# Performance work log

Measured on AMD Instinct MI355X. Metric: run time of the kernel, lower is better.

Reference implementation:

```python
import jax, jax.numpy as jnp
import numpy as np

N_NODES = 10000
N_EDGES = 160000
N_GRAPHS = 20
IN_F, HID, OUT_F, HEADS = 50, 256, 121, 4
NEG_SLOPE = 0.2
GN_EPS = 1e-5
SM_EPS = 1e-16


def _with_self_loops(edge_index, n):
    loop = jnp.arange(n, dtype=edge_index.dtype)
    src = jnp.concatenate([edge_index[0], loop])
    dst = jnp.concatenate([edge_index[1], loop])
    return src, dst


def gat_conv(x, W, att_src, att_dst, bias, src, dst, heads, out_c):
    # PyG GATConv: linear -> per-node attention halves -> edge leaky_relu
    # -> softmax over incoming edges of each dst -> weighted scatter-sum.
    n = x.shape[0]
    h = (x @ W).reshape(n, heads, out_c)                # [N,H,C]
    a_s = (h * att_src).sum(-1)                          # [N,H]
    a_d = (h * att_dst).sum(-1)                          # [N,H]
    e = a_s[src] + a_d[dst]                              # [E,H]
    e = jnp.where(e > 0, e, NEG_SLOPE * e)
    e_max = jax.ops.segment_max(e, dst, num_segments=n)  # self-loops cover all dst
    ex = jnp.exp(e - e_max[dst])
    den = jax.ops.segment_sum(ex, dst, num_segments=n)
    alpha = ex / (den[dst] + SM_EPS)                     # [E,H]
    out = jax.ops.segment_sum(h[src] * alpha[..., None], dst, num_segments=n)
    return out.reshape(n, heads * out_c) + bias


def graph_norm(x, batch, weight, bias, mean_scale, n_graphs):
    cnt = jax.ops.segment_sum(jnp.ones((x.shape[0],), x.dtype), batch,
                              num_segments=n_graphs)[:, None]    # [G,1]
    mean = jax.ops.segment_sum(x, batch, num_segments=n_graphs) / cnt
    ctr = x - mean[batch] * mean_scale
    var = jax.ops.segment_sum(ctr * ctr, batch, num_segments=n_graphs) / cnt
    inv = jax.lax.rsqrt(var + GN_EPS)
    return weight * ctr * inv[batch] + bias


def setup_inputs() -> dict:
    key = jax.random.key(0)
    ks = jax.random.split(key, 24)
    d = {}
    d['x'] = jax.random.normal(ks[0], (N_NODES, IN_F), jnp.float32)
    d['edge_index'] = jax.random.randint(ks[1], (2, N_EDGES), 0, N_NODES, jnp.int64 if jax.config.jax_enable_x64 else jnp.int32)
    d['batch'] = jnp.sort(jax.random.randint(ks[2], (N_NODES,), 0, N_GRAPHS))
    def glorot(k, shape):
        fan = shape[0] + shape[-1]
        return jax.random.normal(k, shape, jnp.float32) * np.sqrt(2.0 / fan)
    dims = [(IN_F, HEADS, HID), (HEADS * HID, HEADS, HID), (HEADS * HID, HEADS, HID), (HEADS * HID, 1, OUT_F)]
    i = 3
    for li, (fin, h, c) in enumerate(dims, 1):
        d[f'W{li}'] = glorot(ks[i], (fin, h * c)); i += 1
        d[f'as{li}'] = glorot(ks[i], (h, c)); i += 1
        d[f'ad{li}'] = glorot(ks[i], (h, c)); i += 1
        d[f'b{li}'] = jnp.zeros((h * c,), jnp.float32)
    for li in (1, 2, 3):
        w = HEADS * HID
        d[f'gw{li}'] = jnp.ones((w,), jnp.float32)
        d[f'gb{li}'] = jnp.zeros((w,), jnp.float32)
        d[f'ga{li}'] = jnp.ones((w,), jnp.float32)
    return d


def reference(x, edge_index, batch,
              W1, as1, ad1, b1, W2, as2, ad2, b2, W3, as3, ad3, b3, W4, as4, ad4, b4,
              gw1, gb1, ga1, gw2, gb2, ga2, gw3, gb3, ga3):
    src, dst = _with_self_loops(edge_index, N_NODES)
    h = gat_conv(x, W1, as1, ad1, b1, src, dst, HEADS, HID)
    h = jax.nn.elu(graph_norm(h, batch, gw1, gb1, ga1, N_GRAPHS))
    h = gat_conv(h, W2, as2, ad2, b2, src, dst, HEADS, HID)
    h = jax.nn.elu(graph_norm(h, batch, gw2, gb2, ga2, N_GRAPHS))
    h = gat_conv(h, W3, as3, ad3, b3, src, dst, HEADS, HID)
    h = jax.nn.elu(graph_norm(h, batch, gw3, gb3, ga3, N_GRAPHS))
    return gat_conv(h, W4, as4, ad4, b4, src, dst, 1, OUT_F)
```

## Files before the change

### kernel.cpp

```cpp
#include <hip/hip_runtime.h>
#include <math.h>

#define NN 10000
#define NE 160000
#define E2 (NE + NN)
#define NG 20
#define MPAD 10240
#define NSPLIT 8

typedef __attribute__((ext_vector_type(8))) short short8;
typedef __attribute__((ext_vector_type(4))) float f32x4;
typedef __attribute__((ext_vector_type(4))) unsigned short us4;

__device__ inline unsigned short f2bf(float f){
  unsigned u = __float_as_uint(f);
  unsigned r = u + 0x7FFFu + ((u >> 16) & 1u);
  return (unsigned short)(r >> 16);
}
__device__ inline float bf2f(unsigned short h){ return __uint_as_float(((unsigned)h) << 16); }

__device__ inline void gload_lds16(const void* g, void* l){
  __builtin_amdgcn_global_load_lds((const __attribute__((address_space(1))) void*)g,
                                   (__attribute__((address_space(3))) void*)l, 16, 0, 0);
}

__global__ void k_gptr(const int* __restrict__ batch, int* __restrict__ gptr){
  int g = threadIdx.x;
  if (g > NG) return;
  int lo = 0, hi = NN;
  while (lo < hi){ int mid = (lo+hi)>>1; if (batch[mid] < g) lo = mid+1; else hi = mid; }
  gptr[g] = lo;
}

__global__ void k_count(const int* __restrict__ ei, int* __restrict__ cnt){
  int e = blockIdx.x*256 + threadIdx.x;
  if (e >= E2) return;
  int d = (e < NE) ? ei[NE + e] : (e - NE);
  atomicAdd(&cnt[d], 1);
}

__global__ void k_scan(const int* __restrict__ cnt, int* __restrict__ ptr){
  __shared__ int tpre[256];
  __shared__ int tsum[256];
  int tid = threadIdx.x;
  const int per = (NN + 255)/256;
  int base = tid*per;
  int s = 0;
  for (int i=0;i<per;i++){ int idx=base+i; if (idx<NN) s += cnt[idx]; }
  tsum[tid] = s;
  __syncthreads();
  if (tid == 0){
    int run = 0;
    for (int i=0;i<256;i++){ tpre[i]=run; run += tsum[i]; }
    ptr[NN] = run;
  }
  __syncthreads();
  int run = tpre[tid];
  for (int i=0;i<per;i++){ int idx=base+i; if (idx<NN){ ptr[idx]=run; run += cnt[idx]; } }
}

__global__ void k_copy(const int* __restrict__ src, int* __restrict__ dst){
  int i = blockIdx.x*256 + threadIdx.x;
  if (i < NN) dst[i] = src[i];
}

__global__ void k_scatter(const int* __restrict__ ei, int* __restrict__ fill, int* __restrict__ csrc){
  int e = blockIdx.x*256 + threadIdx.x;
  if (e >= E2) return;
  int s, d;
  if (e < NE){ s = ei[e]; d = ei[NE + e]; } else { s = d = e - NE; }
  int pos = atomicAdd(&fill[d], 1);
  csrc[pos] = s;
}

__global__ void k_xconv(const float* __restrict__ x, unsigned short* __restrict__ xbf){
  int i = blockIdx.x*256 + threadIdx.x;
  if (i >= MPAD*64) return;
  int r = i >> 6, c = i & 63;
  float v = (r < NN && c < 50) ? x[r*50 + c] : 0.f;
  xbf[i] = f2bf(v);
}

#define WT0 0
#define WT1 65536
#define WT2 1114112
#define WT3 2162688
#define WTT 2293760
__global__ void k_wconvall(const float* __restrict__ W0, const float* __restrict__ W1,
                           const float* __restrict__ W2, const float* __restrict__ W3,
                           unsigned short* __restrict__ wt){
  int i = blockIdx.x*256 + threadIdx.x;
  if (i >= WTT) return;
  const float* W; int K, N, Kpad, off;
  if (i < WT1){ W=W0; K=50; N=1024; Kpad=64; off=WT0; }
  else if (i < WT2){ W=W1; K=1024; N=1024; Kpad=1024; off=WT1; }
  else if (i < WT3){ W=W2; K=1024; N=1024; Kpad=1024; off=WT2; }
  else { W=W3; K=1024; N=121; Kpad=1024; off=WT3; }
  int j = i - off;
  int nn = j / Kpad, kk = j - nn*Kpad;
  float v = (nn < N && kk < K) ? W[(size_t)kk*N + nn] : 0.f;
  wt[i] = f2bf(v);
}

__global__ void k_attpad4(const float* __restrict__ AS3, const float* __restrict__ AD3,
                          float* __restrict__ asp4, float* __restrict__ adp4){
  int i = threadIdx.x;
  asp4[i] = (i < 121) ? AS3[i] : 0.f;
  adp4[i] = (i < 121) ? AD3[i] : 0.f;
}

template<int TBM, int TBN>
__global__ __launch_bounds__(512, 4) void k_gemm256(
    const unsigned short* __restrict__ A,
    const unsigned short* __restrict__ Bt,
    unsigned short* __restrict__ Cbf,
    const float* __restrict__ asp, const float* __restrict__ adp,
    float* __restrict__ a_s, float* __restrict__ a_d,
    int M, int K, int FS, int ncb, int H)
{
  constexpr int MFR = TBM/32;
  constexpr int NFR = TBN/64;
  constexpr int ABYTES = TBM*64;
  constexpr int BBYTES = TBN*64;
  constexpr int AINST = TBM/128;
  constexpr int BINST = TBN/128;
  constexpr int LPS = AINST + BINST;
  __shared__ unsigned short sA[3*TBM*32];
  __shared__ unsigned short sB[3*TBN*32];
  const int tid = threadIdx.x;
  const int wave = tid >> 6;
  const int lane = tid & 63;
  const int nwg = gridDim.x;
  const int q = nwg >> 3, rmod = nwg & 7;
  const int xcd = blockIdx.x & 7, idx = blockIdx.x >> 3;
  const int wg = (xcd < rmod) ? (xcd*(q+1) + idx) : (rmod*(q+1) + (xcd - rmod)*q + idx);
  const int rowt = wg / ncb;
  const int colt = wg - rowt*ncb;
  const int row0 = rowt * TBM;
  const int col0 = colt * TBN;
  const int wr = (wave >> 2) * (TBM/2);
  const int wc = (wave & 3) * (TBN/4);
  f32x4 acc[MFR][NFR];
  #pragma unroll
  for (int i=0;i<MFR;i++)
    #pragma unroll
    for (int j=0;j<NFR;j++){ acc[i][j][0]=0.f; acc[i][j][1]=0.f; acc[i][j][2]=0.f; acc[i][j][3]=0.f; }

  const unsigned short* aP[AINST];
  int aL[AINST];
  #pragma unroll
  for (int i=0;i<AINST;i++){
    int s = (wave*AINST + i)*64 + lane;
    int row = s >> 2, chn = (s & 3) ^ ((row >> 1) & 3);
    aP[i] = A + (size_t)(row0 + row)*K + chn*8;
    aL[i] = (wave*AINST + i)*1024;
  }
  const unsigned short* bP[BINST];
  int bL[BINST];
  #pragma unroll
  for (int i=0;i<BINST;i++){
    int s = (wave*BINST + i)*64 + lane;
    int row = s >> 2, chn = (s & 3) ^ ((row >> 1) & 3);
    bP[i] = Bt + (size_t)(col0 + row)*K + chn*8;
    bL[i] = (wave*BINST + i)*1024;
  }
  char* ldsA = (char*)sA;
  char* ldsB = (char*)sB;

  auto STAGE = [&](int k0, int buf){
    #pragma unroll
    for (int i=0;i<AINST;i++) gload_lds16(aP[i] + k0, ldsA + buf*ABYTES + aL[i]);
    #pragma unroll
    for (int i=0;i<BINST;i++) gload_lds16(bP[i] + k0, ldsB + buf*BBYTES + bL[i]);
  };

  const int NT = K >> 5;
  const int kch = lane >> 4;
  const int rlo = lane & 15;

  STAGE(0, 0);
  STAGE(32, 1);

  int cur = 0;
  for (int t = 0; t < NT; ++t){
    asm volatile("s_waitcnt lgkmcnt(0)" ::: "memory");
    if (t+1 < NT){
      if constexpr (LPS==4)      asm volatile("s_waitcnt vmcnt(4)" ::: "memory");
      else if constexpr (LPS==3) asm volatile("s_waitcnt vmcnt(3)" ::: "memory");
      else                       asm volatile("s_waitcnt vmcnt(2)" ::: "memory");
    } else {
      asm volatile("s_waitcnt vmcnt(0)" ::: "memory");
    }
    __builtin_amdgcn_sched_barrier(0);
    __builtin_amdgcn_s_barrier();
    __builtin_amdgcn_sched_barrier(0);
    const unsigned short* bA = sA + cur*(TBM*32);
    const unsigned short* bB = sB + cur*(TBN*32);
    short8 af[MFR], bfr[NFR];
    #pragma unroll
    for (int m=0;m<MFR;m++){
      int r = wr + m*16 + rlo;
      af[m] = *(const short8*)(bA + r*32 + ((kch ^ ((r>>1)&3))<<3));
    }
    #pragma unroll
    for (int n=0;n<NFR;n++){
      int r = wc + n*16 + rlo;
      bfr[n] = *(const short8*)(bB + r*32 + ((kch ^ ((r>>1)&3))<<3));
    }
    if (t+2 < NT){
      int nb = cur + 2; if (nb >= 3) nb -= 3;
      STAGE((t+2) << 5, nb);
    }
    __builtin_amdgcn_s_setprio(1);
    #pragma unroll
    for (int m=0;m<MFR;m++)
      #pragma unroll
      for (int n=0;n<NFR;n++)
        acc[m][n] = __builtin_amdgcn_mfma_f32_16x16x32_bf16(af[m], bfr[n], acc[m][n], 0, 0, 0);
    __builtin_amdgcn_s_setprio(0);
    cur += 1; if (cur == 3) cur = 0;
  }
  const int cr = (lane >> 4) * 4;
  const int cc = lane & 15;
  #pragma unroll
  for (int m=0;m<MFR;m++){
    #pragma unroll
    for (int n=0;n<NFR;n++){
      int col = col0 + wc + n*16 + cc;
      #pragma unroll
      for (int r=0;r<4;r++){
        int row = row0 + wr + m*16 + cr + r;
        if (row < M) Cbf[(size_t)row*FS + col] = f2bf(acc[m][n][r]);
      }
    }
  }
  float asv[NFR], adv[NFR];
  #pragma unroll
  for (int n=0;n<NFR;n++){
    int col = col0 + wc + n*16 + cc;
    asv[n] = asp[col]; adv[n] = adp[col];
  }
  __syncthreads();
  float* part = (float*)sA;
  #pragma unroll
  for (int m=0;m<MFR;m++){
    #pragma unroll
    for (int r=0;r<4;r++){
      float ss = 0.f, sd = 0.f;
      #pragma unroll
      for (int n=0;n<NFR;n++){ float v = acc[m][n][r]; ss += v*asv[n]; sd += v*adv[n]; }
      #pragma unroll
      for (int o=8;o;o>>=1){ ss += __shfl_xor(ss,o); sd += __shfl_xor(sd,o); }
      if (cc == 0){
        int rowLocal = m*16 + cr + r;
        int pidx = ((wave>>2)*(TBM/2) + rowLocal)*8 + (wave&3)*2;
        part[pidx] = ss; part[pidx+1] = sd;
      }
    }
  }
  __syncthreads();
  if (tid < TBM*2){
    int row = tid >> 1, v = tid & 1;
    int base = row*8 + v;
    float s = part[base] + part[base+2] + part[base+4] + part[base+6];
    int grow = row0 + row;
    const int head = colt;
    if (grow < M){
      if (v) a_d[grow*H + head] = s;
      else   a_s[grow*H + head] = s;
    }
  }
}

__global__ __launch_bounds__(256) void k_gatherw(
    const unsigned short* __restrict__ h,
    const float* __restrict__ a_s, const float* __restrict__ a_d,
    const int* __restrict__ ptr, const int* __restrict__ csrc,
    const float* __restrict__ bias, float* __restrict__ out)
{
  __shared__ float sal[4][64*4];
  __shared__ int ssn[4][64];
  const int wid = threadIdx.x >> 6, lane = threadIdx.x & 63;
  const int node = blockIdx.x*4 + wid;
  const int hh = lane >> 4;
  const int beg = ptr[node], deg = ptr[node+1] - beg;
  f32x4 ad4 = *(const f32x4*)(a_d + node*4);
  float acc[16], acc2[16];
  #pragma unroll
  for (int j=0;j<16;j++){ acc[j]=0.f; acc2[j]=0.f; }
  f32x4 denp = {0.f,0.f,0.f,0.f};
  const unsigned short* hb = h + lane*16;

  for (int c0 = 0; c0 < deg; c0 += 64){
    int n = min(64, deg - c0);
    if (lane < n){
      int s = csrc[beg + c0 + lane];
      f32x4 as4 = *(const f32x4*)(a_s + s*4);
      f32x4 e4;
      #pragma unroll
      for (int k2=0;k2<4;k2++){
        float ev = as4[k2] + ad4[k2];
        ev = ev > 0.f ? ev : 0.2f*ev;
        float x = __expf(ev);
        e4[k2] = x;
        denp[k2] += x;
      }
      *(f32x4*)&sal[wid][lane*4] = e4;
      ssn[wid][lane] = s;
    }
    int e = 0;
    if (n >= 2){
      int s0 = ssn[wid][0], s1 = ssn[wid][1];
      float aA = sal[wid][hh], aB = sal[wid][4+hh];
      const unsigned short* p0 = hb + (size_t)s0*1024;
      const unsigned short* p1 = hb + (size_t)s1*1024;
      short8 ca0=*(const short8*)p0, ca1=*(const short8*)(p0+8);
      short8 cb0=*(const short8*)p1, cb1=*(const short8*)(p1+8);
      for (e = 0; e+3 < n; e += 2){
        int s2 = ssn[wid][e+2], s3 = ssn[wid][e+3];
        float nA = sal[wid][(e+2)*4+hh], nB = sal[wid][(e+3)*4+hh];
        const unsigned short* p2 = hb + (size_t)s2*1024;
        const unsigned short* p3 = hb + (size_t)s3*1024;
        short8 na0=*(const short8*)p2, na1=*(const short8*)(p2+8);
        short8 nb0=*(const short8*)p3, nb1=*(const short8*)(p3+8);
        #pragma unroll
        for (int j=0;j<8;j++){ acc[j]   += bf2f((unsigned short)ca0[j])*aA;
                               acc[8+j] += bf2f((unsigned short)ca1[j])*aA; }
        #pragma unroll
        for (int j=0;j<8;j++){ acc2[j]   += bf2f((unsigned short)cb0[j])*aB;
                               acc2[8+j] += bf2f((unsigned short)cb1[j])*aB; }
        ca0=na0; ca1=na1; cb0=nb0; cb1=nb1; aA=nA; aB=nB;
      }
      #pragma unroll
      for (int j=0;j<8;j++){ acc[j]   += bf2f((unsigned short)ca0[j])*aA;
                             acc[8+j] += bf2f((unsigned short)ca1[j])*aA; }
      #pragma unroll
      for (int j=0;j<8;j++){ acc2[j]   += bf2f((unsigned short)cb0[j])*aB;
                             acc2[8+j] += bf2f((unsigned short)cb1[j])*aB; }
      e += 2;
    }
    for (; e < n; ++e){
      int s = ssn[wid][e];
      float al = sal[wid][e*4 + hh];
      const unsigned short* p = hb + (size_t)s*1024;
      short8 u0 = *(const short8*)p, u1 = *(const short8*)(p+8);
      #pragma unroll
      for (int j=0;j<8;j++){ acc[j]   += bf2f((unsigned short)u0[j])*al;
                             acc[8+j] += bf2f((unsigned short)u1[j])*al; }
    }
  }
  #pragma unroll
  for (int o=32;o;o>>=1){
    #pragma unroll
    for (int k2=0;k2<4;k2++) denp[k2] += __shfl_xor(denp[k2], o);
  }
  float inv = 1.f / (denp[hh] + 1e-16f);
  float* op = out + (size_t)node*1024 + lane*16;
  const float* bp = bias + lane*16;
  #pragma unroll
  for (int j=0;j<16;j++) op[j] = (acc[j]+acc2[j])*inv + bp[j];
}

__global__ __launch_bounds__(256) void k_gatherw1(
    const unsigned short* __restrict__ h,
    const float* __restrict__ a_s, const float* __restrict__ a_d,
    const int* __restrict__ ptr, const int* __restrict__ csrc,
    const float* __restrict__ bias, float* __restrict__ out)
{
  __shared__ float sal[4][64];
  __shared__ int ssn[4][64];
  const int wid = threadIdx.x >> 6, lane = threadIdx.x & 63;
  const int node = blockIdx.x*4 + wid;
  const int beg = ptr[node], deg = ptr[node+1] - beg;
  float ad = a_d[node];
  float den = 0.f;
  float acc[2] = {0.f,0.f}, acc2[2] = {0.f,0.f};
  const int c0i = lane*2;
  const unsigned short* hb = h + c0i;

  for (int b0 = 0; b0 < deg; b0 += 64){
    int n = min(64, deg - b0);
    if (lane < n){
      int s = csrc[beg + b0 + lane];
      float ev = a_s[s] + ad;
      ev = ev > 0.f ? ev : 0.2f*ev;
      float x = __expf(ev);
      sal[wid][lane] = x;
      ssn[wid][lane] = s;
      den += x;
    }
    int e = 0;
    for (; e + 1 < n; e += 2){
      int sA_ = ssn[wid][e], sB_ = ssn[wid][e+1];
      float aA = sal[wid][e], aB = sal[wid][e+1];
      const unsigned short* pA = hb + (size_t)sA_*128;
      const unsigned short* pB = hb + (size_t)sB_*128;
      acc[0]  += bf2f(pA[0])*aA; acc[1]  += bf2f(pA[1])*aA;
      acc2[0] += bf2f(pB[0])*aB; acc2[1] += bf2f(pB[1])*aB;
    }
    if (e < n){
      int sA_ = ssn[wid][e];
      float aA = sal[wid][e];
      const unsigned short* pA = hb + (size_t)sA_*128;
      acc[0] += bf2f(pA[0])*aA; acc[1] += bf2f(pA[1])*aA;
    }
  }
  #pragma unroll
  for (int o=32;o;o>>=1) den += __shfl_xor(den, o);
  float inv = 1.f / (den + 1e-16f);
  if (c0i < 121)   out[(size_t)node*121 + c0i]   = (acc[0]+acc2[0])*inv + bias[c0i];
  if (c0i+1 < 121) out[(size_t)node*121 + c0i+1] = (acc[1]+acc2[1])*inv + bias[c0i+1];
}

__global__ void k_gnstats(const float* __restrict__ x, const int* __restrict__ gptr,
                          float* __restrict__ psum, float* __restrict__ psq){
  int g = blockIdx.x, sp = blockIdx.z;
  int c4 = threadIdx.x*4;
  int beg = gptr[g], end = gptr[g+1];
  int n = end - beg;
  int per = (n + NSPLIT - 1) / NSPLIT;
  int nb = beg + sp*per, ne = min(end, nb + per);
  f32x4 s = {0.f,0.f,0.f,0.f}, qv = {0.f,0.f,0.f,0.f};
  for (int i = nb; i < ne; i++){
    f32x4 v = *(const f32x4*)(x + (size_t)i*1024 + c4);
    s += v; qv += v*v;
  }
  int idx = (sp*NG + g)*1024 + c4;
  *(f32x4*)(psum + idx) = s;
  *(f32x4*)(psq + idx) = qv;
}

__global__ void k_coef(const float* __restrict__ psum, const float* __restrict__ psq,
                       const int* __restrict__ gptr,
                       const float* __restrict__ w, const float* __restrict__ b, const float* __restrict__ ms,
                       float* __restrict__ cA, float* __restrict__ cB){
  int i = blockIdx.x*256 + threadIdx.x;
  if (i >= NG*1024) return;
  int g = i >> 10, c = i & 1023;
  float cntf = (float)(gptr[g+1] - gptr[g]);
  float sm = 0.f, sq = 0.f;
  #pragma unroll
  for (int sp=0; sp<NSPLIT; sp++){
    sm += psum[(sp*NG + g)*1024 + c];
    sq += psq[(sp*NG + g)*1024 + c];
  }
  float m = sm / cntf;
  float s = ms[c];
  float ex2 = sq / cntf;
  float var = ex2 - 2.f*s*m*m + s*s*m*m;
  float inv = rsqrtf(var + 1e-5f);
  float wa = w[c]*inv;
  cA[i] = wa;
  cB[i] = b[c] - wa*m*s;
}

__global__ void k_applyelu(const float* __restrict__ x, const int* __restrict__ batch,
                           const float* __restrict__ cA, const float* __restrict__ cB,
                           unsigned short* __restrict__ obf){
  int i = blockIdx.x*256 + threadIdx.x;
  if (i >= NN*256) return;
  int node = i >> 8;
  int c4 = (i & 255)*4;
  int g = batch[node];
  f32x4 v = *(const f32x4*)(x + (size_t)node*1024 + c4);
  f32x4 a = *(const f32x4*)(cA + g*1024 + c4);
  f32x4 b = *(const f32x4*)(cB + g*1024 + c4);
  us4 o;
  #pragma unroll
  for (int j=0;j<4;j++){
    float y = a[j]*v[j] + b[j];
    y = y > 0.f ? y : expm1f(y);
    o[j] = f2bf(y);
  }
  *(us4*)(obf + (size_t)node*1024 + c4) = o;
}

extern "C" void kernel_launch(void* const* d_in, const int* in_sizes, int n_in,
                              void* d_out, int out_size, void* d_ws, size_t ws_size,
                              hipStream_t stream){
  (void)in_sizes; (void)n_in; (void)out_size; (void)ws_size;
  const float* x     = (const float*)d_in[0];
  const int*   ei    = (const int*)d_in[1];
  const int*   batch = (const int*)d_in[2];
  const float* W[4]  = {(const float*)d_in[3],  (const float*)d_in[7],  (const float*)d_in[11], (const float*)d_in[15]};
  const float* AS[4] = {(const float*)d_in[4],  (const float*)d_in[8],  (const float*)d_in[12], (const float*)d_in[16]};
  const float* AD[4] = {(const float*)d_in[5],  (const float*)d_in[9],  (const float*)d_in[13], (const float*)d_in[17]};
  const float* BI[4] = {(const float*)d_in[6],  (const float*)d_in[10], (const float*)d_in[14], (const float*)d_in[18]};
  const float* GW[3] = {(const float*)d_in[19], (const float*)d_in[22], (const float*)d_in[25]};
  const float* GB[3] = {(const float*)d_in[20], (const float*)d_in[23], (const float*)d_in[26]};
  const float* GA[3] = {(const float*)d_in[21], (const float*)d_in[24], (const float*)d_in[27]};

  float* ws   = (float*)d_ws;
  float* bufB = ws;
  float* a_s  = bufB + (size_t)NN*1024;
  float* a_d  = a_s + (size_t)NN*4;
  float* psum = a_d + (size_t)NN*4;
  float* psq  = psum + (size_t)NSPLIT*NG*1024;
  float* cA   = psq  + (size_t)NSPLIT*NG*1024;
  float* cB   = cA   + (size_t)NG*1024;
  float* asp4 = cB   + (size_t)NG*1024;
  float* adp4 = asp4 + 128;
  int* ptr  = (int*)(adp4 + 128);
  int* fill = ptr + (NN + 8);
  int* csrc = fill + (NN + 8);
  int* gptr = csrc + E2;
  unsigned short* abf = (unsigned short*)(gptr + 24);
  unsigned short* xbf = abf;
  unsigned short* hbf = abf + (size_t)MPAD*1024;
  unsigned short* wt  = hbf + (size_t)NN*1024;

  hipMemsetAsync(fill, 0, sizeof(int)*(NN+1), stream);
  k_gptr<<<1, 32, 0, stream>>>(batch, gptr);
  k_count<<<(E2+255)/256, 256, 0, stream>>>(ei, fill);
  k_scan<<<1, 256, 0, stream>>>(fill, ptr);
  k_copy<<<(NN+255)/256, 256, 0, stream>>>(ptr, fill);
  k_scatter<<<(E2+255)/256, 256, 0, stream>>>(ei, fill, csrc);
  k_xconv<<<(MPAD*64+255)/256, 256, 0, stream>>>(x, xbf);
  k_wconvall<<<(WTT+255)/256, 256, 0, stream>>>(W[0], W[1], W[2], W[3], wt);
  k_attpad4<<<1, 128, 0, stream>>>(AS[3], AD[3], asp4, adp4);

  const int Kp[4]  = {64, 1024, 1024, 1024};
  const int Np[4]  = {1024, 1024, 1024, 128};
  const int Woff[4] = {WT0, WT1, WT2, WT3};
  for (int li = 0; li < 4; ++li){
    int FS = Np[li];
    const unsigned short* Ain = (li == 0) ? xbf : abf;
    const unsigned short* Wt = wt + Woff[li];
    if (li < 3){
      int ncb = 4;
      int nwg = (MPAD/128) * ncb;
      k_gemm256<128,256><<<nwg, 512, 0, stream>>>(Ain, Wt, hbf, AS[li], AD[li], a_s, a_d,
                                                  NN, Kp[li], FS, ncb, 4);
      k_gatherw<<<NN/4, 256, 0, stream>>>(hbf, a_s, a_d, ptr, csrc, BI[li], bufB);
      k_gnstats<<<dim3(NG, 1, NSPLIT), 256, 0, stream>>>(bufB, gptr, psum, psq);
      k_coef<<<(NG*1024 + 255)/256, 256, 0, stream>>>(psum, psq, gptr, GW[li], GB[li], GA[li], cA, cB);
      k_applyelu<<<(NN*256 + 255)/256, 256, 0, stream>>>(bufB, batch, cA, cB, abf);
    } else {
      int ncb = 1;
      int nwg = (MPAD/256) * ncb;
      k_gemm256<256,128><<<nwg, 512, 0, stream>>>(Ain, Wt, hbf, asp4, adp4, a_s, a_d,
                                                  NN, Kp[li], FS, ncb, 1);
      k_gatherw1<<<NN/4, 256, 0, stream>>>(hbf, a_s, a_d, ptr, csrc, BI[li], (float*)d_out);
    }
  }
}
```

Measured before the change: 482.4 us.

## Merge setup kernels, shrink last-layer GEMM tile, widen gather loads, more GN splits

Folds the x conversion, weight conversion and attention padding kernels into one setup launch to cut launch overhead. The final layer GEMM moves to a 128x128 tile so twice as many workgroups cover the 10240 padded rows. The layer-4 gather reads two bf16 values with one 32-bit load instead of two 16-bit loads. The GraphNorm stats split goes from 8 to 16 to raise parallelism. The 128x128 template instantiation is untested here and may interact differently with the GEMM epilogue.

After: 445.5 us. 1.08x faster.

```diff
diff --git a/kernel.cpp b/kernel.cpp
--- a/kernel.cpp
+++ b/kernel.cpp
@@ -6,7 +6,7 @@
 #define E2 (NE + NN)
 #define NG 20
 #define MPAD 10240
-#define NSPLIT 8
+#define NSPLIT 16
 
 typedef __attribute__((ext_vector_type(8))) short short8;
 typedef __attribute__((ext_vector_type(4))) float f32x4;
@@ -73,40 +73,39 @@
   csrc[pos] = s;
 }
 
-__global__ void k_xconv(const float* __restrict__ x, unsigned short* __restrict__ xbf){
-  int i = blockIdx.x*256 + threadIdx.x;
-  if (i >= MPAD*64) return;
-  int r = i >> 6, c = i & 63;
-  float v = (r < NN && c < 50) ? x[r*50 + c] : 0.f;
-  xbf[i] = f2bf(v);
-}
-
 #define WT0 0
 #define WT1 65536
 #define WT2 1114112
 #define WT3 2162688
 #define WTT 2293760
-__global__ void k_wconvall(const float* __restrict__ W0, const float* __restrict__ W1,
-                           const float* __restrict__ W2, const float* __restrict__ W3,
-                           unsigned short* __restrict__ wt){
+#define XS  (MPAD*64)
+__global__ void k_setup(const float* __restrict__ W0, const float* __restrict__ W1,
+                        const float* __restrict__ W2, const float* __restrict__ W3,
+                        const float* __restrict__ x,
+                        const float* __restrict__ AS3, const float* __restrict__ AD3,
+                        unsigned short* __restrict__ wt, unsigned short* __restrict__ xbf,
+                        float* __restrict__ asp4, float* __restrict__ adp4){
   int i = blockIdx.x*256 + threadIdx.x;
-  if (i >= WTT) return;
-  const float* W; int K, N, Kpad, off;
-  if (i < WT1){ W=W0; K=50; N=1024; Kpad=64; off=WT0; }
-  else if (i < WT2){ W=W1; K=1024; N=1024; Kpad=1024; off=WT1; }
-  else if (i < WT3){ W=W2; K=1024; N=1024; Kpad=1024; off=WT2; }
-  else { W=W3; K=1024; N=121; Kpad=1024; off=WT3; }
-  int j = i - off;
-  int nn = j / Kpad, kk = j - nn*Kpad;
-  float v = (nn < N && kk < K) ? W[(size_t)kk*N + nn] : 0.f;
-  wt[i] = f2bf(v);
-}
-
-__global__ void k_attpad4(const float* __restrict__ AS3, const float* __restrict__ AD3,
-                          float* __restrict__ asp4, float* __restrict__ adp4){
-  int i = threadIdx.x;
-  asp4[i] = (i < 121) ? AS3[i] : 0.f;
-  adp4[i] = (i < 121) ? AD3[i] : 0.f;
+  if (i < WTT){
+    const float* W; int K, N, Kpad, off;
+    if (i < WT1){ W=W0; K=50; N=1024; Kpad=64; off=WT0; }
+    else if (i < WT2){ W=W1; K=1024; N=1024; Kpad=1024; off=WT1; }
+    else if (i < WT3){ W=W2; K=1024; N=1024; Kpad=1024; off=WT2; }
+    else { W=W3; K=1024; N=121; Kpad=1024; off=WT3; }
+    int j = i - off;
+    int nn = j / Kpad, kk = j - nn*Kpad;
+    float v = (nn < N && kk < K) ? W[(size_t)kk*N + nn] : 0.f;
+    wt[i] = f2bf(v);
+  } else if (i < WTT + XS){
+    int j = i - WTT;
+    int r = j >> 6, c = j & 63;
+    float v = (r < NN && c < 50) ? x[r*50 + c] : 0.f;
+    xbf[j] = f2bf(v);
+  } else if (i < WTT + XS + 128){
+    int j = i - WTT - XS;
+    asp4[j] = (j < 121) ? AS3[j] : 0.f;
+    adp4[j] = (j < 121) ? AD3[j] : 0.f;
+  }
 }
 
 template<int TBM, int TBN>
@@ -393,16 +392,19 @@
     for (; e + 1 < n; e += 2){
       int sA_ = ssn[wid][e], sB_ = ssn[wid][e+1];
       float aA = sal[wid][e], aB = sal[wid][e+1];
-      const unsigned short* pA = hb + (size_t)sA_*128;
-      const unsigned short* pB = hb + (size_t)sB_*128;
-      acc[0]  += bf2f(pA[0])*aA; acc[1]  += bf2f(pA[1])*aA;
-      acc2[0] += bf2f(pB[0])*aB; acc2[1] += bf2f(pB[1])*aB;
+      unsigned uA = *(const unsigned*)(hb + (size_t)sA_*128);
+      unsigned uB = *(const unsigned*)(hb + (size_t)sB_*128);
+      acc[0]  += bf2f((unsigned short)(uA & 0xFFFF))*aA;
+      acc[1]  += bf2f((unsigned short)(uA >> 16))*aA;
+      acc2[0] += bf2f((unsigned short)(uB & 0xFFFF))*aB;
+      acc2[1] += bf2f((unsigned short)(uB >> 16))*aB;
     }
     if (e < n){
       int sA_ = ssn[wid][e];
       float aA = sal[wid][e];
-      const unsigned short* pA = hb + (size_t)sA_*128;
-      acc[0] += bf2f(pA[0])*aA; acc[1] += bf2f(pA[1])*aA;
+      unsigned uA = *(const unsigned*)(hb + (size_t)sA_*128);
+      acc[0] += bf2f((unsigned short)(uA & 0xFFFF))*aA;
+      acc[1] += bf2f((unsigned short)(uA >> 16))*aA;
     }
   }
   #pragma unroll
@@ -515,9 +517,8 @@
   k_scan<<<1, 256, 0, stream>>>(fill, ptr);
   k_copy<<<(NN+255)/256, 256, 0, stream>>>(ptr, fill);
   k_scatter<<<(E2+255)/256, 256, 0, stream>>>(ei, fill, csrc);
-  k_xconv<<<(MPAD*64+255)/256, 256, 0, stream>>>(x, xbf);
-  k_wconvall<<<(WTT+255)/256, 256, 0, stream>>>(W[0], W[1], W[2], W[3], wt);
-  k_attpad4<<<1, 128, 0, stream>>>(AS[3], AD[3], asp4, adp4);
+  k_setup<<<(WTT + XS + 128 + 255)/256, 256, 0, stream>>>(W[0], W[1], W[2], W[3], x,
+                                                          AS[3], AD[3], wt, xbf, asp4, adp4);
 
   const int Kp[4]  = {64, 1024, 1024, 1024};
   const int Np[4]  = {1024, 1024, 1024, 128};
@@ -537,8 +538,8 @@
       k_applyelu<<<(NN*256 + 255)/256, 256, 0, stream>>>(bufB, batch, cA, cB, abf);
     } else {
       int ncb = 1;
-      int nwg = (MPAD/256) * ncb;
-      k_gemm256<256,128><<<nwg, 512, 0, stream>>>(Ain, Wt, hbf, asp4, adp4, a_s, a_d,
+      int nwg = (MPAD/128) * ncb;
+      k_gemm256<128,128><<<nwg, 512, 0, stream>>>(Ain, Wt, hbf, asp4, adp4, a_s, a_d,
                                                   NN, Kp[li], FS, ncb, 1);
       k_gatherw1<<<NN/4, 256, 0, stream>>>(hbf, a_s, a_d, ptr, csrc, BI[li], (float*)d_out);
     }
```
